# Kernel tuning notes

Measured on AMD Instinct MI355X. Metric: run time of the kernel, lower is better.

The kernel has to match this reference:

```python
import jax, jax.numpy as jnp
import numpy as np

N = 100000
E = 3200000
D_IN = 128
D_OUT = 128
ALPHA = 0.2  # LeakyReLU negative slope
LN_EPS = 1e-5


def setup_inputs() -> dict:
    key = jax.random.key(0)
    k1, k2, k3, k4, k5 = jax.random.split(key, 5)
    x = jax.random.normal(k1, (N, D_IN), dtype=jnp.float32)
    edge = jax.random.randint(k2, (2, E), 0, N, dtype=jnp.int64)
    # Linear params (kaiming-normal-ish init)
    W = jax.random.normal(k3, (D_OUT, D_IN), dtype=jnp.float32) * np.sqrt(2.0 / D_IN)
    b = jnp.zeros((D_OUT,), dtype=jnp.float32)
    # attention vector a: (2*out,)
    a = jax.random.normal(k4, (2 * D_OUT,), dtype=jnp.float32) * np.sqrt(2.0 / (2 * D_OUT))
    ln_w = jnp.ones((D_OUT,), dtype=jnp.float32)
    ln_b = jnp.zeros((D_OUT,), dtype=jnp.float32)
    return {"x": x, "W": W, "b": b, "a": a, "ln_w": ln_w, "ln_b": ln_b, "edge": edge}


def reference(x, W, b, a, ln_w, ln_b, edge):
    n = x.shape[0]
    d_out = W.shape[0]
    h = x @ W.T + b  # [N, D_OUT]
    src, dst = edge[0], edge[1]
    # a.mm(cat(h[src], h[dst]).T) == h[src] @ a1 + h[dst] @ a2
    a1, a2 = a[:d_out], a[d_out:]
    node_s1 = h @ a1  # [N]
    node_s2 = h @ a2  # [N]
    z = node_s1[src] + node_s2[dst]  # [E]
    edge_e = jnp.exp(-jax.nn.leaky_relu(z, ALPHA))  # [E]
    # sparse spmm: h_prime[i] = sum_{e: src=i} edge_e[e] * h[dst[e]]
    msgs = edge_e[:, None] * h[dst]  # [E, D_OUT]
    h_prime = jax.ops.segment_sum(msgs, src, num_segments=n)  # [N, D_OUT]
    # LayerNorm over last dim
    mu = jnp.mean(h_prime, axis=-1, keepdims=True)
    var = jnp.mean(jnp.square(h_prime - mu), axis=-1, keepdims=True)
    h_norm = (h_prime - mu) * jax.lax.rsqrt(var + LN_EPS) * ln_w + ln_b
    return jax.nn.elu(h_norm)
```

## Files before the change

kernel.cpp:

```cpp
#include <hip/hip_runtime.h>
#include <math.h>

#define D 128
#define GAT_ALPHA 0.2f
#define LN_EPS 1e-5f
#define BSHIFT 5
#define BKT 32
#define NBMAX 3200
#define CAPB 1280
#define ECHUNK 16384
#define XPITCH 136

typedef __attribute__((ext_vector_type(8))) short short8;
typedef __attribute__((ext_vector_type(4))) float floatx4;

__device__ __forceinline__ unsigned short f2bf(float f) {
    unsigned u = __float_as_uint(f);
    unsigned r = (u + 0x7fffu + ((u >> 16) & 1u)) >> 16;
    return (unsigned short)r;
}
__device__ __forceinline__ float bfl(unsigned u) { return __uint_as_float(u << 16); }
__device__ __forceinline__ float bfh(unsigned u) { return __uint_as_float(u & 0xffff0000u); }

union SmemU {
    struct { unsigned short Bf[16384]; unsigned short xs[128 * XPITCH]; } g;
    struct { int cnt[NBMAX]; int basex[NBMAX]; int cnt2x[NBMAX]; } p;
};

__global__ __launch_bounds__(512) void gemm_partition(
        const float* __restrict__ x, const float* __restrict__ W,
        const float* __restrict__ b, const float* __restrict__ a,
        const int* __restrict__ src, const int* __restrict__ dst,
        int* __restrict__ gcnt, int* __restrict__ pairs,
        unsigned short* __restrict__ h16, float* __restrict__ s1,
        float* __restrict__ s2, int n, int nE, int nb, int npart)
{
    __shared__ SmemU sm;
    const int tid = threadIdx.x;

    if (blockIdx.x < npart) {
        int* cnt = sm.p.cnt; int* basex = sm.p.basex; int* cnt2x = sm.p.cnt2x;
        for (int i = tid; i < nb; i += 512) { cnt[i] = 0; cnt2x[i] = 0; }
        __syncthreads();
        int e0 = blockIdx.x * ECHUNK;
        int e1 = e0 + ECHUNK; if (e1 > nE) e1 = nE;
        for (int e = e0 + tid; e < e1; e += 512)
            atomicAdd(&cnt[src[e] >> BSHIFT], 1);
        __syncthreads();
        for (int i = tid; i < nb; i += 512)
            basex[i] = cnt[i] ? atomicAdd(&gcnt[i], cnt[i]) : 0;
        __syncthreads();
        for (int e = e0 + tid; e < e1; e += 512) {
            int s = src[e];
            int bb = s >> BSHIFT;
            int l = basex[bb] + atomicAdd(&cnt2x[bb], 1);
            if (l < CAPB) pairs[(size_t)bb * CAPB + l] = ((s & (BKT - 1)) << 24) | dst[e];
        }
        return;
    }

    unsigned short* Bf = sm.g.Bf;
    unsigned short* xs = sm.g.xs;

    for (int idx = tid; idx < 2048; idx += 512) {
        int lane = idx & 63, ntkt = idx >> 6;
        int nt = ntkt >> 2, kt = ntkt & 3;
        int bl16 = lane & 15, bquad = lane >> 4;
        const float* wp = W + (size_t)(nt * 16 + bl16) * D + kt * 32 + bquad * 8;
        float4 w0 = *(const float4*)wp;
        float4 w1 = *(const float4*)(wp + 4);
        ushort4 o0, o1;
        o0.x = f2bf(w0.x); o0.y = f2bf(w0.y); o0.z = f2bf(w0.z); o0.w = f2bf(w0.w);
        o1.x = f2bf(w1.x); o1.y = f2bf(w1.y); o1.z = f2bf(w1.z); o1.w = f2bf(w1.w);
        *(ushort4*)&Bf[idx * 8]     = o0;
        *(ushort4*)&Bf[idx * 8 + 4] = o1;
    }

    const int lane = tid & 63, wave = tid >> 6;
    const int l16 = lane & 15, quad = lane >> 4;
    const int row0 = (blockIdx.x - npart) * 128;

    for (int i = tid; i < 4096; i += 512) {
        int row = i >> 5, c4 = i & 31;
        float4 v = make_float4(0.f, 0.f, 0.f, 0.f);
        if (row0 + row < n) v = *(const float4*)(x + (size_t)(row0 + row) * D + c4 * 4);
        ushort4 o;
        o.x = f2bf(v.x); o.y = f2bf(v.y); o.z = f2bf(v.z); o.w = f2bf(v.w);
        *(ushort4*)&xs[row * XPITCH + c4 * 4] = o;
    }

    float bcol[8], a1c[8], a2c[8];
#pragma unroll
    for (int nt = 0; nt < 8; ++nt) {
        int c = nt * 16 + l16;
        bcol[nt] = b[c]; a1c[nt] = a[c]; a2c[nt] = a[D + c];
    }
    __syncthreads();

    floatx4 acc[8];
#pragma unroll
    for (int nt = 0; nt < 8; ++nt) acc[nt] = (floatx4){0.f, 0.f, 0.f, 0.f};

#pragma unroll
    for (int kt = 0; kt < 4; ++kt) {
        short8 af = *(const short8*)&xs[(wave * 16 + l16) * XPITCH + kt * 32 + quad * 8];
#pragma unroll
        for (int nt = 0; nt < 8; ++nt) {
            short8 bf = *(const short8*)&Bf[(size_t)((nt * 4 + kt) * 64 + lane) * 8];
            acc[nt] = __builtin_amdgcn_mfma_f32_16x16x32_bf16(af, bf, acc[nt], 0, 0, 0);
        }
    }

    float hv[4][8];
#pragma unroll
    for (int r = 0; r < 4; ++r) {
        float p1 = 0.f, p2 = 0.f;
#pragma unroll
        for (int nt = 0; nt < 8; ++nt) {
            float v = acc[nt][r] + bcol[nt];
            hv[r][nt] = v;
            p1 = fmaf(v, a1c[nt], p1);
            p2 = fmaf(v, a2c[nt], p2);
        }
#pragma unroll
        for (int off = 8; off > 0; off >>= 1) {
            p1 += __shfl_xor(p1, off);
            p2 += __shfl_xor(p2, off);
        }
        int crow = row0 + wave * 16 + quad * 4 + r;
        if (crow < n && l16 == 0) { s1[crow] = p1; s2[crow] = p2; }
    }

    __syncthreads();
#pragma unroll
    for (int r = 0; r < 4; ++r)
#pragma unroll
        for (int nt = 0; nt < 8; ++nt)
            xs[(wave * 16 + quad * 4 + r) * XPITCH + nt * 16 + l16] = f2bf(hv[r][nt]);
    __syncthreads();

    for (int i = tid; i < 2048; i += 512) {
        int row = i >> 4, c = i & 15;
        if (row0 + row < n)
            *(uint4*)(h16 + (size_t)(row0 + row) * D + c * 8) =
                *(const uint4*)&xs[row * XPITCH + c * 8];
    }
}

__global__ __launch_bounds__(128, 6) void sort_aggregate(const int* __restrict__ pairs,
                                                         const int* __restrict__ gcnt,
                                                         const float* __restrict__ s1,
                                                         const float* __restrict__ s2,
                                                         const unsigned short* __restrict__ h16,
                                                         const float* __restrict__ ln_w,
                                                         const float* __restrict__ ln_b,
                                                         float* __restrict__ out, int n)
{
    __shared__ int2 csr2[CAPB];
    __shared__ int cnt[BKT], cnt2[BKT], excl[BKT + 1];
    __shared__ float sA[BKT];

    const int bkt = blockIdx.x, tid = threadIdx.x;
    const size_t base = (size_t)bkt * CAPB;
    int m = gcnt[bkt]; if (m > CAPB) m = CAPB;

    if (tid < BKT) {
        cnt[tid] = 0; cnt2[tid] = 0;
        int node = bkt * BKT + tid;
        sA[tid] = (node < n) ? s1[node] : 0.f;
    }
    __syncthreads();

    for (int e = tid; e < m; e += 128)
        atomicAdd(&cnt[((unsigned)pairs[base + e]) >> 24], 1);
    __syncthreads();

    if (tid < 32) {
        int v = cnt[tid], incl = v;
#pragma unroll
        for (int off = 1; off < 32; off <<= 1) {
            int t = __shfl_up(incl, off);
            if (tid >= off) incl += t;
        }
        excl[tid] = incl - v;
        if (tid == 31) excl[32] = incl;
    }
    __syncthreads();

    for (int e = tid; e < m; e += 128) {
        int w = pairs[base + e];
        int sl = ((unsigned)w) >> 24;
        int d = w & 0xFFFFFF;
        float z = sA[sl] + s2[d];
        float lz = z > 0.f ? z : GAT_ALPHA * z;
        float ee = __expf(-lz);
        int pos = excl[sl] + atomicAdd(&cnt2[sl], 1);
        csr2[pos] = make_int2(d, __float_as_int(ee));
    }
    __syncthreads();

    const int gq = tid >> 4;
    const int l16 = tid & 15;

#pragma unroll 1
    for (int i = 0; i < BKT / 8; ++i) {
        int nl = i * 8 + gq;
        int node = bkt * BKT + nl;
        bool alive = node < n;
        int e0 = alive ? excl[nl] : 0;
        int e1 = alive ? excl[nl + 1] : 0;

        float acc[8];
#pragma unroll
        for (int j = 0; j < 8; ++j) acc[j] = 0.f;

        int e = e0;
        for (; e + 3 < e1; e += 4) {
            int2 pa = csr2[e];
            int2 pb = csr2[e + 1];
            int2 pc = csr2[e + 2];
            int2 pd = csr2[e + 3];
            uint4 ua = *(const uint4*)(h16 + (size_t)pa.x * D + l16 * 8);
            uint4 ub = *(const uint4*)(h16 + (size_t)pb.x * D + l16 * 8);
            uint4 uc = *(const uint4*)(h16 + (size_t)pc.x * D + l16 * 8);
            uint4 ud = *(const uint4*)(h16 + (size_t)pd.x * D + l16 * 8);
            float ea = __int_as_float(pa.y);
            float eb = __int_as_float(pb.y);
            float ec = __int_as_float(pc.y);
            float ed = __int_as_float(pd.y);
            acc[0] = fmaf(ea, bfl(ua.x), acc[0]);
            acc[1] = fmaf(ea, bfh(ua.x), acc[1]);
            acc[2] = fmaf(ea, bfl(ua.y), acc[2]);
            acc[3] = fmaf(ea, bfh(ua.y), acc[3]);
            acc[4] = fmaf(ea, bfl(ua.z), acc[4]);
            acc[5] = fmaf(ea, bfh(ua.z), acc[5]);
            acc[6] = fmaf(ea, bfl(ua.w), acc[6]);
            acc[7] = fmaf(ea, bfh(ua.w), acc[7]);
            acc[0] = fmaf(eb, bfl(ub.x), acc[0]);
            acc[1] = fmaf(eb, bfh(ub.x), acc[1]);
            acc[2] = fmaf(eb, bfl(ub.y), acc[2]);
            acc[3] = fmaf(eb, bfh(ub.y), acc[3]);
            acc[4] = fmaf(eb, bfl(ub.z), acc[4]);
            acc[5] = fmaf(eb, bfh(ub.z), acc[5]);
            acc[6] = fmaf(eb, bfl(ub.w), acc[6]);
            acc[7] = fmaf(eb, bfh(ub.w), acc[7]);
            acc[0] = fmaf(ec, bfl(uc.x), acc[0]);
            acc[1] = fmaf(ec, bfh(uc.x), acc[1]);
            acc[2] = fmaf(ec, bfl(uc.y), acc[2]);
            acc[3] = fmaf(ec, bfh(uc.y), acc[3]);
            acc[4] = fmaf(ec, bfl(uc.z), acc[4]);
            acc[5] = fmaf(ec, bfh(uc.z), acc[5]);
            acc[6] = fmaf(ec, bfl(uc.w), acc[6]);
            acc[7] = fmaf(ec, bfh(uc.w), acc[7]);
            acc[0] = fmaf(ed, bfl(ud.x), acc[0]);
            acc[1] = fmaf(ed, bfh(ud.x), acc[1]);
            acc[2] = fmaf(ed, bfl(ud.y), acc[2]);
            acc[3] = fmaf(ed, bfh(ud.y), acc[3]);
            acc[4] = fmaf(ed, bfl(ud.z), acc[4]);
            acc[5] = fmaf(ed, bfh(ud.z), acc[5]);
            acc[6] = fmaf(ed, bfl(ud.w), acc[6]);
            acc[7] = fmaf(ed, bfh(ud.w), acc[7]);
        }
        for (; e < e1; ++e) {
            int2 p = csr2[e];
            float ee = __int_as_float(p.y);
            uint4 u = *(const uint4*)(h16 + (size_t)p.x * D + l16 * 8);
            acc[0] = fmaf(ee, bfl(u.x), acc[0]);
            acc[1] = fmaf(ee, bfh(u.x), acc[1]);
            acc[2] = fmaf(ee, bfl(u.y), acc[2]);
            acc[3] = fmaf(ee, bfh(u.y), acc[3]);
            acc[4] = fmaf(ee, bfl(u.z), acc[4]);
            acc[5] = fmaf(ee, bfh(u.z), acc[5]);
            acc[6] = fmaf(ee, bfl(u.w), acc[6]);
            acc[7] = fmaf(ee, bfh(u.w), acc[7]);
        }

        float sum = 0.f, sq = 0.f;
#pragma unroll
        for (int j = 0; j < 8; ++j) { sum += acc[j]; sq += acc[j] * acc[j]; }
#pragma unroll
        for (int off = 8; off > 0; off >>= 1) {
            sum += __shfl_xor(sum, off);
            sq  += __shfl_xor(sq, off);
        }

        if (alive) {
            float mu   = sum * (1.0f / 128.0f);
            float var  = sq * (1.0f / 128.0f) - mu * mu;
            float rstd = rsqrtf(var + LN_EPS);

            float4 w0 = *(const float4*)(ln_w + l16 * 8);
            float4 w1 = *(const float4*)(ln_w + l16 * 8 + 4);
            float4 b0 = *(const float4*)(ln_b + l16 * 8);
            float4 b1 = *(const float4*)(ln_b + l16 * 8 + 4);
            float y[8];
            y[0] = (acc[0] - mu) * rstd * w0.x + b0.x;
            y[1] = (acc[1] - mu) * rstd * w0.y + b0.y;
            y[2] = (acc[2] - mu) * rstd * w0.z + b0.z;
            y[3] = (acc[3] - mu) * rstd * w0.w + b0.w;
            y[4] = (acc[4] - mu) * rstd * w1.x + b1.x;
            y[5] = (acc[5] - mu) * rstd * w1.y + b1.y;
            y[6] = (acc[6] - mu) * rstd * w1.z + b1.z;
            y[7] = (acc[7] - mu) * rstd * w1.w + b1.w;
#pragma unroll
            for (int j = 0; j < 8; ++j) y[j] = y[j] > 0.f ? y[j] : expm1f(y[j]);
            float* op = out + (size_t)node * D + l16 * 8;
            *(float4*)op       = make_float4(y[0], y[1], y[2], y[3]);
            *(float4*)(op + 4) = make_float4(y[4], y[5], y[6], y[7]);
        }
    }
}

extern "C" void kernel_launch(void* const* d_in, const int* in_sizes, int n_in,
                              void* d_out, int out_size, void* d_ws, size_t ws_size,
                              hipStream_t stream)
{
    const float* x    = (const float*)d_in[0];
    const float* W    = (const float*)d_in[1];
    const float* b    = (const float*)d_in[2];
    const float* a    = (const float*)d_in[3];
    const float* ln_w = (const float*)d_in[4];
    const float* ln_b = (const float*)d_in[5];
    const int*   edge = (const int*)d_in[6];

    const int n  = in_sizes[0] / D;
    const int nE = in_sizes[6] / 2;
    const int* src = edge;
    const int* dst = edge + nE;
    const int nb = (n + BKT - 1) >> BSHIFT;
    const int npart = (nE + ECHUNK - 1) / ECHUNK;
    const int ngemm = (n + 127) / 128;

    float* out = (float*)d_out;

    unsigned short* h16 = (unsigned short*)d_ws;
    float* s1   = (float*)(h16 + (size_t)n * D);
    float* s2   = s1 + n;
    int* pairs  = (int*)(s2 + n);
    int* gcnt   = pairs + (size_t)nb * CAPB;

    hipMemsetAsync(gcnt, 0, (size_t)nb * sizeof(int), stream);

    gemm_partition<<<npart + ngemm, 512, 0, stream>>>(x, W, b, a, src, dst,
                                                      gcnt, pairs, h16, s1, s2,
                                                      n, nE, nb, npart);
    sort_aggregate<<<nb, 128, 0, stream>>>(pairs, gcnt, s1, s2, h16, ln_w, ln_b, out, n);
}
```

Measured before the change: 322.6 us.

## Halve bucket size to 16 nodes, use 64-thread blocks, unroll gather by 8

Buckets now hold 16 destination nodes instead of 32. There are twice as many sort_aggregate blocks, each of 64 threads, and the per-bucket edge capacity and partition chunk size change to match. The gather loop now issues 8 independent row loads per iteration instead of 4, to raise memory-level parallelism. This gives finer work granularity and better load balance, at the cost of more blocks, more global atomics on bucket counters in partitioning, and a tighter per-bucket capacity (704) that could overflow for high-degree buckets.

After: 433.1 us. +34.3%, slower.

```diff
diff --git a/kernel.cpp b/kernel.cpp
--- a/kernel.cpp
+++ b/kernel.cpp
@@ -4,11 +4,11 @@
 #define D 128
 #define GAT_ALPHA 0.2f
 #define LN_EPS 1e-5f
-#define BSHIFT 5
-#define BKT 32
-#define NBMAX 3200
-#define CAPB 1280
-#define ECHUNK 16384
+#define BSHIFT 4
+#define BKT 16
+#define NBMAX 6400
+#define CAPB 704
+#define ECHUNK 32768
 #define XPITCH 136
 
 typedef __attribute__((ext_vector_type(8))) short short8;
@@ -147,14 +147,14 @@
     }
 }
 
-__global__ __launch_bounds__(128, 6) void sort_aggregate(const int* __restrict__ pairs,
-                                                         const int* __restrict__ gcnt,
-                                                         const float* __restrict__ s1,
-                                                         const float* __restrict__ s2,
-                                                         const unsigned short* __restrict__ h16,
-                                                         const float* __restrict__ ln_w,
-                                                         const float* __restrict__ ln_b,
-                                                         float* __restrict__ out, int n)
+__global__ __launch_bounds__(64, 7) void sort_aggregate(const int* __restrict__ pairs,
+                                                        const int* __restrict__ gcnt,
+                                                        const float* __restrict__ s1,
+                                                        const float* __restrict__ s2,
+                                                        const unsigned short* __restrict__ h16,
+                                                        const float* __restrict__ ln_w,
+                                                        const float* __restrict__ ln_b,
+                                                        float* __restrict__ out, int n)
 {
     __shared__ int2 csr2[CAPB];
     __shared__ int cnt[BKT], cnt2[BKT], excl[BKT + 1];
@@ -171,23 +171,23 @@
     }
     __syncthreads();
 
-    for (int e = tid; e < m; e += 128)
+    for (int e = tid; e < m; e += 64)
         atomicAdd(&cnt[((unsigned)pairs[base + e]) >> 24], 1);
     __syncthreads();
 
-    if (tid < 32) {
+    if (tid < BKT) {
         int v = cnt[tid], incl = v;
 #pragma unroll
-        for (int off = 1; off < 32; off <<= 1) {
+        for (int off = 1; off < BKT; off <<= 1) {
             int t = __shfl_up(incl, off);
             if (tid >= off) incl += t;
         }
         excl[tid] = incl - v;
-        if (tid == 31) excl[32] = incl;
-    }
-    __syncthreads();
-
-    for (int e = tid; e < m; e += 128) {
+        if (tid == BKT - 1) excl[BKT] = incl;
+    }
+    __syncthreads();
+
+    for (int e = tid; e < m; e += 64) {
         int w = pairs[base + e];
         int sl = ((unsigned)w) >> 24;
         int d = w & 0xFFFFFF;
@@ -203,8 +203,8 @@
     const int l16 = tid & 15;
 
 #pragma unroll 1
-    for (int i = 0; i < BKT / 8; ++i) {
-        int nl = i * 8 + gq;
+    for (int i = 0; i < BKT / 4; ++i) {
+        int nl = i * 4 + gq;
         int node = bkt * BKT + nl;
         bool alive = node < n;
         int e0 = alive ? excl[nl] : 0;
@@ -215,65 +215,45 @@
         for (int j = 0; j < 8; ++j) acc[j] = 0.f;
 
         int e = e0;
-        for (; e + 3 < e1; e += 4) {
-            int2 pa = csr2[e];
-            int2 pb = csr2[e + 1];
-            int2 pc = csr2[e + 2];
-            int2 pd = csr2[e + 3];
-            uint4 ua = *(const uint4*)(h16 + (size_t)pa.x * D + l16 * 8);
-            uint4 ub = *(const uint4*)(h16 + (size_t)pb.x * D + l16 * 8);
-            uint4 uc = *(const uint4*)(h16 + (size_t)pc.x * D + l16 * 8);
-            uint4 ud = *(const uint4*)(h16 + (size_t)pd.x * D + l16 * 8);
-            float ea = __int_as_float(pa.y);
-            float eb = __int_as_float(pb.y);
-            float ec = __int_as_float(pc.y);
-            float ed = __int_as_float(pd.y);
-            acc[0] = fmaf(ea, bfl(ua.x), acc[0]);
-            acc[1] = fmaf(ea, bfh(ua.x), acc[1]);
-            acc[2] = fmaf(ea, bfl(ua.y), acc[2]);
-            acc[3] = fmaf(ea, bfh(ua.y), acc[3]);
-            acc[4] = fmaf(ea, bfl(ua.z), acc[4]);
-            acc[5] = fmaf(ea, bfh(ua.z), acc[5]);
-            acc[6] = fmaf(ea, bfl(ua.w), acc[6]);
-            acc[7] = fmaf(ea, bfh(ua.w), acc[7]);
-            acc[0] = fmaf(eb, bfl(ub.x), acc[0]);
-            acc[1] = fmaf(eb, bfh(ub.x), acc[1]);
-            acc[2] = fmaf(eb, bfl(ub.y), acc[2]);
-            acc[3] = fmaf(eb, bfh(ub.y), acc[3]);
-            acc[4] = fmaf(eb, bfl(ub.z), acc[4]);
-            acc[5] = fmaf(eb, bfh(ub.z), acc[5]);
-            acc[6] = fmaf(eb, bfl(ub.w), acc[6]);
-            acc[7] = fmaf(eb, bfh(ub.w), acc[7]);
-            acc[0] = fmaf(ec, bfl(uc.x), acc[0]);
-            acc[1] = fmaf(ec, bfh(uc.x), acc[1]);
-            acc[2] = fmaf(ec, bfl(uc.y), acc[2]);
-            acc[3] = fmaf(ec, bfh(uc.y), acc[3]);
-            acc[4] = fmaf(ec, bfl(uc.z), acc[4]);
-            acc[5] = fmaf(ec, bfh(uc.z), acc[5]);
-            acc[6] = fmaf(ec, bfl(uc.w), acc[6]);
-            acc[7] = fmaf(ec, bfh(uc.w), acc[7]);
-            acc[0] = fmaf(ed, bfl(ud.x), acc[0]);
-            acc[1] = fmaf(ed, bfh(ud.x), acc[1]);
-            acc[2] = fmaf(ed, bfl(ud.y), acc[2]);
-            acc[3] = fmaf(ed, bfh(ud.y), acc[3]);
-            acc[4] = fmaf(ed, bfl(ud.z), acc[4]);
-            acc[5] = fmaf(ed, bfh(ud.z), acc[5]);
-            acc[6] = fmaf(ed, bfl(ud.w), acc[6]);
-            acc[7] = fmaf(ed, bfh(ud.w), acc[7]);
-        }
-        for (; e < e1; ++e) {
-            int2 p = csr2[e];
-            float ee = __int_as_float(p.y);
-            uint4 u = *(const uint4*)(h16 + (size_t)p.x * D + l16 * 8);
-            acc[0] = fmaf(ee, bfl(u.x), acc[0]);
-            acc[1] = fmaf(ee, bfh(u.x), acc[1]);
-            acc[2] = fmaf(ee, bfl(u.y), acc[2]);
-            acc[3] = fmaf(ee, bfh(u.y), acc[3]);
-            acc[4] = fmaf(ee, bfl(u.z), acc[4]);
-            acc[5] = fmaf(ee, bfh(u.z), acc[5]);
-            acc[6] = fmaf(ee, bfl(u.w), acc[6]);
-            acc[7] = fmaf(ee, bfh(u.w), acc[7]);
-        }
+        for (; e + 7 < e1; e += 8) {
+            int2 p0 = csr2[e];     int2 p1 = csr2[e + 1];
+            int2 p2 = csr2[e + 2]; int2 p3 = csr2[e + 3];
+            int2 p4 = csr2[e + 4]; int2 p5 = csr2[e + 5];
+            int2 p6 = csr2[e + 6]; int2 p7 = csr2[e + 7];
+            uint4 u0 = *(const uint4*)(h16 + (size_t)p0.x * D + l16 * 8);
+            uint4 u1 = *(const uint4*)(h16 + (size_t)p1.x * D + l16 * 8);
+            uint4 u2 = *(const uint4*)(h16 + (size_t)p2.x * D + l16 * 8);
+            uint4 u3 = *(const uint4*)(h16 + (size_t)p3.x * D + l16 * 8);
+            uint4 u4 = *(const uint4*)(h16 + (size_t)p4.x * D + l16 * 8);
+            uint4 u5 = *(const uint4*)(h16 + (size_t)p5.x * D + l16 * 8);
+            uint4 u6 = *(const uint4*)(h16 + (size_t)p6.x * D + l16 * 8);
+            uint4 u7 = *(const uint4*)(h16 + (size_t)p7.x * D + l16 * 8);
+            float w0 = __int_as_float(p0.y), w1 = __int_as_float(p1.y);
+            float w2 = __int_as_float(p2.y), w3 = __int_as_float(p3.y);
+            float w4 = __int_as_float(p4.y), w5 = __int_as_float(p5.y);
+            float w6 = __int_as_float(p6.y), w7 = __int_as_float(p7.y);
+#define ACC8(W, U) \
+            acc[0] = fmaf(W, bfl(U.x), acc[0]); acc[1] = fmaf(W, bfh(U.x), acc[1]); \
+            acc[2] = fmaf(W, bfl(U.y), acc[2]); acc[3] = fmaf(W, bfh(U.y), acc[3]); \
+            acc[4] = fmaf(W, bfl(U.z), acc[4]); acc[5] = fmaf(W, bfh(U.z), acc[5]); \
+            acc[6] = fmaf(W, bfl(U.w), acc[6]); acc[7] = fmaf(W, bfh(U.w), acc[7]);
+            ACC8(w0, u0) ACC8(w1, u1) ACC8(w2, u2) ACC8(w3, u3)
+            ACC8(w4, u4) ACC8(w5, u5) ACC8(w6, u6) ACC8(w7, u7)
+        }
+        for (; e + 1 < e1; e += 2) {
+            int2 p0 = csr2[e]; int2 p1 = csr2[e + 1];
+            uint4 u0 = *(const uint4*)(h16 + (size_t)p0.x * D + l16 * 8);
+            uint4 u1 = *(const uint4*)(h16 + (size_t)p1.x * D + l16 * 8);
+            float w0 = __int_as_float(p0.y), w1 = __int_as_float(p1.y);
+            ACC8(w0, u0) ACC8(w1, u1)
+        }
+        if (e < e1) {
+            int2 p0 = csr2[e];
+            uint4 u0 = *(const uint4*)(h16 + (size_t)p0.x * D + l16 * 8);
+            float w0 = __int_as_float(p0.y);
+            ACC8(w0, u0)
+        }
+#undef ACC8
 
         float sum = 0.f, sq = 0.f;
 #pragma unroll
@@ -344,5 +324,5 @@
     gemm_partition<<<npart + ngemm, 512, 0, stream>>>(x, W, b, a, src, dst,
                                                       gcnt, pairs, h16, s1, s2,
                                                       n, nE, nb, npart);
-    sort_aggregate<<<nb, 128, 0, stream>>>(pairs, gcnt, s1, s2, h16, ln_w, ln_b, out, n);
+    sort_aggregate<<<nb, 64, 0, stream>>>(pairs, gcnt, s1, s2, h16, ln_w, ln_b, out, n);
 }
```

## Split fused GEMM/partition kernel and use direct global atomics for edge bucketing

Applied to the files above, without the earlier changes.

Separates the combined GEMM+edge-partition kernel into two launches: a standalone MFMA GEMM and a simple one-thread-per-edge scatter that takes bucket slots with global atomicAdd on gcnt. This removes the shared-memory histogram and two-pass counting per chunk, along with the large union LDS footprint that capped occupancy for the GEMM blocks. In exchange it issues about 3.2M global atomics onto roughly 3125 counters, which can contend heavily, and the GEMM and partition no longer overlap within one launch.

Result: slower. 534.0 us (+65.5%).

```diff
diff --git a/kernel.cpp b/kernel.cpp
--- a/kernel.cpp
+++ b/kernel.cpp
@@ -6,9 +6,7 @@
 #define LN_EPS 1e-5f
 #define BSHIFT 5
 #define BKT 32
-#define NBMAX 3200
 #define CAPB 1280
-#define ECHUNK 16384
 #define XPITCH 136
 
 typedef __attribute__((ext_vector_type(8))) short short8;
@@ -22,45 +20,15 @@
 __device__ __forceinline__ float bfl(unsigned u) { return __uint_as_float(u << 16); }
 __device__ __forceinline__ float bfh(unsigned u) { return __uint_as_float(u & 0xffff0000u); }
 
-union SmemU {
-    struct { unsigned short Bf[16384]; unsigned short xs[128 * XPITCH]; } g;
-    struct { int cnt[NBMAX]; int basex[NBMAX]; int cnt2x[NBMAX]; } p;
-};
-
-__global__ __launch_bounds__(512) void gemm_partition(
+__global__ __launch_bounds__(512) void gemm_mfma(
         const float* __restrict__ x, const float* __restrict__ W,
         const float* __restrict__ b, const float* __restrict__ a,
-        const int* __restrict__ src, const int* __restrict__ dst,
-        int* __restrict__ gcnt, int* __restrict__ pairs,
         unsigned short* __restrict__ h16, float* __restrict__ s1,
-        float* __restrict__ s2, int n, int nE, int nb, int npart)
+        float* __restrict__ s2, int n)
 {
-    __shared__ SmemU sm;
+    __shared__ unsigned short Bf[16384];
+    __shared__ unsigned short xs[128 * XPITCH];
     const int tid = threadIdx.x;
-
-    if (blockIdx.x < npart) {
-        int* cnt = sm.p.cnt; int* basex = sm.p.basex; int* cnt2x = sm.p.cnt2x;
-        for (int i = tid; i < nb; i += 512) { cnt[i] = 0; cnt2x[i] = 0; }
-        __syncthreads();
-        int e0 = blockIdx.x * ECHUNK;
-        int e1 = e0 + ECHUNK; if (e1 > nE) e1 = nE;
-        for (int e = e0 + tid; e < e1; e += 512)
-            atomicAdd(&cnt[src[e] >> BSHIFT], 1);
-        __syncthreads();
-        for (int i = tid; i < nb; i += 512)
-            basex[i] = cnt[i] ? atomicAdd(&gcnt[i], cnt[i]) : 0;
-        __syncthreads();
-        for (int e = e0 + tid; e < e1; e += 512) {
-            int s = src[e];
-            int bb = s >> BSHIFT;
-            int l = basex[bb] + atomicAdd(&cnt2x[bb], 1);
-            if (l < CAPB) pairs[(size_t)bb * CAPB + l] = ((s & (BKT - 1)) << 24) | dst[e];
-        }
-        return;
-    }
-
-    unsigned short* Bf = sm.g.Bf;
-    unsigned short* xs = sm.g.xs;
 
     for (int idx = tid; idx < 2048; idx += 512) {
         int lane = idx & 63, ntkt = idx >> 6;
@@ -78,7 +46,7 @@
 
     const int lane = tid & 63, wave = tid >> 6;
     const int l16 = lane & 15, quad = lane >> 4;
-    const int row0 = (blockIdx.x - npart) * 128;
+    const int row0 = blockIdx.x * 128;
 
     for (int i = tid; i < 4096; i += 512) {
         int row = i >> 5, c4 = i & 31;
@@ -145,6 +113,19 @@
             *(uint4*)(h16 + (size_t)(row0 + row) * D + c * 8) =
                 *(const uint4*)&xs[row * XPITCH + c * 8];
     }
+}
+
+__global__ __launch_bounds__(256) void partition_scatter(
+        const int* __restrict__ src, const int* __restrict__ dst,
+        int* __restrict__ gcnt, int* __restrict__ pairs, int nE)
+{
+    int e = blockIdx.x * 256 + threadIdx.x;
+    if (e >= nE) return;
+    int s = src[e];
+    int d = dst[e];
+    int bb = s >> BSHIFT;
+    int l = atomicAdd(&gcnt[bb], 1);
+    if (l < CAPB) pairs[(size_t)bb * CAPB + l] = ((s & (BKT - 1)) << 24) | d;
 }
 
 __global__ __launch_bounds__(128, 6) void sort_aggregate(const int* __restrict__ pairs,
@@ -328,8 +309,6 @@
     const int* src = edge;
     const int* dst = edge + nE;
     const int nb = (n + BKT - 1) >> BSHIFT;
-    const int npart = (nE + ECHUNK - 1) / ECHUNK;
-    const int ngemm = (n + 127) / 128;
 
     float* out = (float*)d_out;
 
@@ -341,8 +320,7 @@
 
     hipMemsetAsync(gcnt, 0, (size_t)nb * sizeof(int), stream);
 
-    gemm_partition<<<npart + ngemm, 512, 0, stream>>>(x, W, b, a, src, dst,
-                                                      gcnt, pairs, h16, s1, s2,
-                                                      n, nE, nb, npart);
-    sort_aggregate<<<nb, 128, 0, stream>>>(pairs, gcnt, s1, s2, h16, ln_w, ln_b, out, n);
-}
+    gemm_mfma        <<<(n + 127) / 128, 256 * 2, 0, stream>>>(x, W, b, a, h16, s1, s2, n);
+    partition_scatter<<<(nE + 255) / 256, 256, 0, stream>>>(src, dst, gcnt, pairs, nE);
+    sort_aggregate   <<<nb, 128, 0, stream>>>(pairs, gcnt, s1, s2, h16, ln_w, ln_b, out, n);
+}
```
